# Performance work log

Hardware: AMD Instinct MI355X
Metric: run time of the kernel (lower is better)

The kernel has to match this reference:

```python
import jax, jax.numpy as jnp
import numpy as np

T = 131072      # sequence length (time steps)
IN = 256        # input_dim (MAX_NEURAL_UNITS)
G = 8           # num_dataset_groups
H = 64          # ssm_io_dim (== ssm_dim)
CTX = 8         # context_dim
P = 32          # complex state size = ssm_dim // 2 (conj_sym=True)
NL = 4          # ssm_num_layers
OUT = 2         # output_dim
DT_MIN, DT_MAX = 1e-3, 1e-1


def setup_inputs() -> dict:
    ks = jax.random.split(jax.random.key(0), 16)
    n = lambda i, shape, s=1.0: jax.random.normal(ks[i], shape, dtype=jnp.float32) * s
    return {
        "x": n(0, (T, IN)),
        "group_idx": 3,
        "enc_w": n(1, (G, H - CTX, IN), 1.0 / np.sqrt(IN)),
        "enc_b": n(2, (G, H - CTX), 0.01),
        "ctx_emb": n(3, (G, CTX)),
        "Lambda_re": -0.5 * jnp.abs(n(4, (NL, P))) - 0.1,   # stable (negative real part)
        "Lambda_im": n(5, (NL, P)) * 3.0,
        "B_re": n(6, (NL, P, H), 1.0 / np.sqrt(H)),
        "B_im": n(7, (NL, P, H), 1.0 / np.sqrt(H)),
        "C_re": n(8, (NL, H, P), 1.0 / np.sqrt(P)),
        "C_im": n(9, (NL, H, P), 1.0 / np.sqrt(P)),
        "D": n(10, (NL, H)),
        "log_step": jax.random.uniform(ks[11], (NL, P), jnp.float32, np.log(DT_MIN), np.log(DT_MAX)),
        "norm_scale": jnp.ones((NL, H), jnp.float32),
        "norm_bias": jnp.zeros((NL, H), jnp.float32),
        "glu_w1": n(12, (NL, H, H), 1.0 / np.sqrt(H)),
        "glu_b1": jnp.zeros((NL, H), jnp.float32),
        "glu_w2": n(13, (NL, H, H), 1.0 / np.sqrt(H)),
        "glu_b2": jnp.zeros((NL, H), jnp.float32),
        "dec_w": n(14, (OUT, H), 1.0 / np.sqrt(H)),
        "dec_b": jnp.zeros((OUT,), jnp.float32),
    }


def _s5_scan(Lbar, Bu):
    """Linear recurrence x_k = Lbar * x_{k-1} + Bu_k via parallel associative scan."""
    A = jnp.broadcast_to(Lbar, Bu.shape)  # (T, P) complex

    def binop(a, b):
        a1, u1 = a
        a2, u2 = b
        return a2 * a1, a2 * u1 + u2

    _, xs = jax.lax.associative_scan(binop, (A, Bu))
    return xs  # (T, P) complex


def reference(x, group_idx, enc_w, enc_b, ctx_emb, Lambda_re, Lambda_im, B_re, B_im,
              C_re, C_im, D, log_step, norm_scale, norm_bias,
              glu_w1, glu_b1, glu_w2, glu_b2, dec_w, dec_b):
    # group-routed encoder (lax.switch over per-group Linears == gather of weights)
    h = x @ enc_w[group_idx].T + enc_b[group_idx]                         # (T, H-CTX)
    ctx = jnp.broadcast_to(ctx_emb[group_idx], (h.shape[0], CTX))         # (T, CTX)
    h = jnp.concatenate([h, ctx], axis=1)                                 # (T, H)

    for i in range(NL):  # static layer stack
        skip = h
        # batch-norm over the time axis (training-mode batch statistics)
        mu = jnp.mean(h, axis=0)
        var = jnp.var(h, axis=0)
        hn = (h - mu) * jax.lax.rsqrt(var + 1e-5) * norm_scale[i] + norm_bias[i]

        # ZOH discretisation of diagonal complex SSM
        Lam = jax.lax.complex(Lambda_re[i], Lambda_im[i])                 # (P,)
        dt = jnp.exp(log_step[i])                                         # (P,) step_rescale=1
        Lbar = jnp.exp(Lam * dt)                                          # (P,)
        Bt = jax.lax.complex(B_re[i], B_im[i])                            # (P, H)
        Bbar = (((Lbar - 1.0) / Lam)[:, None]) * Bt                       # (P, H)

        Bu = hn.astype(Bbar.dtype) @ Bbar.T                               # (T, P) complex
        xs = _s5_scan(Lbar, Bu)                                           # (T, P)
        Cm = jax.lax.complex(C_re[i], C_im[i])                            # (H, P)
        y = 2.0 * jnp.real(xs @ Cm.T) + hn * D[i]                         # conj_sym output

        # half-GLU nonlinearity + residual (dropout inactive at inference)
        y = jax.nn.gelu(y)
        y = (y @ glu_w1[i].T + glu_b1[i]) * jax.nn.sigmoid(y @ glu_w2[i].T + glu_b2[i])
        h = skip + y

    return h @ dec_w.T + dec_b                                            # (T, OUT)
```

## Files before the change

kernel.cpp:

```cpp
#include <hip/hip_runtime.h>

#define T_LEN   131072
#define IN_DIM  256
#define HD      64
#define PD      32
#define NLAY    4
#define CHUNK   128
#define NBLK    (T_LEN / CHUNK)
#define ASTR    68

typedef __attribute__((ext_vector_type(8))) short bf16x8;
typedef __attribute__((ext_vector_type(4))) float f32x4;

union FragU { uint4 q; bf16x8 v; };

__device__ __forceinline__ unsigned splitpack(float x) {
    unsigned xb = __float_as_uint(x);
    unsigned hb = (xb + 0x8000u) & 0xffff0000u;
    float lf = x - __uint_as_float(hb);
    unsigned lb = (__float_as_uint(lf) + 0x8000u) >> 16;
    return (hb >> 16) | (lb << 16);
}

__device__ __forceinline__ void packAB(float4 a0, float4 a1, bf16x8& hi, bf16x8& lo) {
    unsigned p0 = splitpack(a0.x), p1 = splitpack(a0.y);
    unsigned p2 = splitpack(a0.z), p3 = splitpack(a0.w);
    unsigned p4 = splitpack(a1.x), p5 = splitpack(a1.y);
    unsigned p6 = splitpack(a1.z), p7 = splitpack(a1.w);
    union { bf16x8 v; unsigned u[4]; } H, L;
    H.u[0] = (p0 & 0xffffu) | (p1 << 16);
    H.u[1] = (p2 & 0xffffu) | (p3 << 16);
    H.u[2] = (p4 & 0xffffu) | (p5 << 16);
    H.u[3] = (p6 & 0xffffu) | (p7 << 16);
    L.u[0] = (p0 >> 16) | (p1 & 0xffff0000u);
    L.u[1] = (p2 >> 16) | (p3 & 0xffff0000u);
    L.u[2] = (p4 >> 16) | (p5 & 0xffff0000u);
    L.u[3] = (p6 >> 16) | (p7 & 0xffff0000u);
    hi = H.v; lo = L.v;
}

#define MFMA3(ACC, AH, AL, BH, BL)                                              \
    ACC = __builtin_amdgcn_mfma_f32_16x16x32_bf16(AH, BH, ACC, 0, 0, 0);        \
    ACC = __builtin_amdgcn_mfma_f32_16x16x32_bf16(AH, BL, ACC, 0, 0, 0);        \
    ACC = __builtin_amdgcn_mfma_f32_16x16x32_bf16(AL, BH, ACC, 0, 0, 0);

__device__ __forceinline__ int kmap(int q, int j) {
    return (j < 4) ? (q * 4 + j) : (16 + q * 4 + (j - 4));
}

__global__ __launch_bounds__(512) void ssm_k0a(
    const float* __restrict__ Lre, const float* __restrict__ Lim,
    const float* __restrict__ logstep,
    float* __restrict__ Lbar, float* __restrict__ Ldt, float* __restrict__ stats)
{
    int tid = threadIdx.x;
    if (tid < NLAY * PD) {
        int l = tid >> 5, p = tid & 31;
        float dt = expf(logstep[l * PD + p]);
        float lr = Lre[l * PD + p], li = Lim[l * PD + p];
        float ldr = lr * dt, ldi = li * dt;
        Ldt[tid * 2] = ldr; Ldt[tid * 2 + 1] = ldi;
        float e = expf(ldr);
        float sn, cs; sincosf(ldi, &sn, &cs);
        Lbar[tid * 2] = e * cs; Lbar[tid * 2 + 1] = e * sn;
    }
    if (tid < NLAY * 128) stats[tid] = 0.0f;
}

__global__ __launch_bounds__(256) void ssm_k0b(
    const float* __restrict__ Lre, const float* __restrict__ Lim,
    const float* __restrict__ logstep,
    const float* __restrict__ Bre, const float* __restrict__ Bim,
    const float* __restrict__ Cre, const float* __restrict__ Cim,
    const float* __restrict__ w1, const float* __restrict__ w2,
    const float* __restrict__ enc_w, const int* __restrict__ gptr,
    unsigned* __restrict__ fragE, unsigned* __restrict__ fragL)
{
    int fi = blockIdx.x * 256 + threadIdx.x;
    if (fi >= 10240) return;
    int g = gptr[0];
    int mat, lay = 0, rem;
    unsigned* outp;
    if (fi < 2048) { mat = 0; rem = fi; outp = fragE + rem * 8; }
    else {
        int t = fi - 2048;
        lay = t / 2048;
        int r2 = t % 2048;
        mat = 1 + r2 / 512;
        rem = r2 % 512;
        outp = fragL + ((size_t)(lay * 4 + (mat - 1)) * 512 + rem) * 8;
    }
    int ks = rem / 256;
    int nt = (rem / 64) & 3;
    int lane = rem & 63;
    int q = lane >> 4;
    int n = nt * 16 + (lane & 15);

    float vals[8];
#pragma unroll
    for (int j = 0; j < 8; ++j) {
        int k = ks * 32 + kmap(q, j);
        float v;
        if (mat == 0) {
            v = (n < 56) ? enc_w[(size_t)(g * 56 + n) * IN_DIM + k] : 0.0f;
        } else if (mat == 1) {
            int p = n >> 1;
            float dt = expf(logstep[lay * PD + p]);
            float lr = Lre[lay * PD + p], li = Lim[lay * PD + p];
            float e = expf(lr * dt);
            float sn, cs; sincosf(li * dt, &sn, &cs);
            float den = lr * lr + li * li;
            float nr = e * cs - 1.0f, ni = e * sn;
            float fr = (nr * lr + ni * li) / den, fimag = (ni * lr - nr * li) / den;
            float br = Bre[(lay * PD + p) * HD + k], bi = Bim[(lay * PD + p) * HD + k];
            v = (n & 1) ? (fr * bi + fimag * br) : (fr * br - fimag * bi);
        } else if (mat == 2) {
            int p = k >> 1;
            v = (k & 1) ? -Cim[((size_t)lay * HD + n) * PD + p]
                        :  Cre[((size_t)lay * HD + n) * PD + p];
        } else if (mat == 3) {
            v = w1[((size_t)lay * HD + n) * HD + k];
        } else {
            v = w2[((size_t)lay * HD + n) * HD + k];
        }
        vals[j] = v;
    }
    unsigned p8[8];
#pragma unroll
    for (int j = 0; j < 8; ++j) p8[j] = splitpack(vals[j]);
#pragma unroll
    for (int w = 0; w < 4; ++w) {
        unsigned p0 = p8[2 * w], p1 = p8[2 * w + 1];
        outp[w]     = (p0 & 0xffffu) | (p1 << 16);
        outp[4 + w] = (p0 >> 16) | (p1 & 0xffff0000u);
    }
}

__global__ __launch_bounds__(64) void ssm_k5_reduce(
    const float* __restrict__ part, float* __restrict__ statsL)
{
    int c = blockIdx.x;
    int lane = threadIdx.x;
    float s = 0.0f;
#pragma unroll
    for (int j = 0; j < 4; ++j) {
        float4 v = *(const float4*)&part[c * 1024 + j * 256 + lane * 4];
        s += v.x + v.y + v.z + v.w;
    }
#pragma unroll
    for (int m = 1; m < 64; m <<= 1) s += __shfl_xor(s, m, 64);
    if (lane == 0) statsL[c] = s;
}

__global__ __launch_bounds__(512, 4) void ssm_k1_encoder(
    const float* __restrict__ x, const int* __restrict__ gptr,
    const unsigned* __restrict__ fragE, const float* __restrict__ enc_b,
    const float* __restrict__ ctx_emb,
    float* __restrict__ h, float* __restrict__ part)
{
    __shared__ float sp1[512], sp2[512];
    int tid = threadIdx.x;
    int l = tid & 63, w = tid >> 6;
    int cq = l >> 4, cr = l & 15;
    int g = gptr[0];
    size_t r0 = (size_t)blockIdx.x * 128;
    int arow = 16 * w + cr;
    const float* xrow = &x[(r0 + arow) * IN_DIM];
    const f32x4 fzero = {0.f, 0.f, 0.f, 0.f};

    float4 cur[16];
#pragma unroll
    for (int kt = 0; kt < 4; ++kt)
#pragma unroll
        for (int ks = 0; ks < 2; ++ks) {
            cur[kt * 4 + 2 * ks]     = *(const float4*)&xrow[kt * 64 + ks * 32 + cq * 4];
            cur[kt * 4 + 2 * ks + 1] = *(const float4*)&xrow[kt * 64 + ks * 32 + cq * 4 + 16];
        }

    f32x4 acc[4];
#pragma unroll
    for (int nt = 0; nt < 4; ++nt) acc[nt] = fzero;

#pragma unroll
    for (int kt = 0; kt < 4; ++kt)
#pragma unroll
        for (int ks = 0; ks < 2; ++ks) {
            bf16x8 ah, al;
            packAB(cur[kt * 4 + 2 * ks], cur[kt * 4 + 2 * ks + 1], ah, al);
            int ksg = kt * 2 + ks;
#pragma unroll
            for (int nt = 0; nt < 4; ++nt) {
                const uint4* wf = (const uint4*)&fragE[((size_t)(ksg * 4 + nt) * 64 + l) * 8];
                FragU BH, BL; BH.q = wf[0]; BL.q = wf[1];
                MFMA3(acc[nt], ah, al, BH.v, BL.v);
            }
        }
#pragma unroll
    for (int nt = 0; nt < 4; ++nt) {
        int ch = nt * 16 + cr;
        float eb = (ch < 56) ? enc_b[g * 56 + ch] : 0.0f;
        bool isctx = (ch >= 56);
        float cv = isctx ? ctx_emb[g * 8 + (ch - 56)] : 0.0f;
        float v1 = 0.0f, v2 = 0.0f;
#pragma unroll
        for (int r = 0; r < 4; ++r) {
            float val = isctx ? cv : (acc[nt][r] + eb);
            h[(r0 + 16 * w + 4 * cq + r) * HD + ch] = val;
            v1 += val; v2 += val * val;
        }
        v1 += __shfl_xor(v1, 16, 64); v2 += __shfl_xor(v2, 16, 64);
        v1 += __shfl_xor(v1, 32, 64); v2 += __shfl_xor(v2, 32, 64);
        if (l < 16) { sp1[w * 64 + ch] = v1; sp2[w * 64 + ch] = v2; }
    }
    __syncthreads();
    if (tid < 64) {
        float s1 = 0.0f, s2 = 0.0f;
#pragma unroll
        for (int ww = 0; ww < 8; ++ww) { s1 += sp1[ww * 64 + tid]; s2 += sp2[ww * 64 + tid]; }
        part[tid * 1024 + blockIdx.x]        = s1;
        part[(64 + tid) * 1024 + blockIdx.x] = s2;
    }
}

__global__ __launch_bounds__(512, 4) void ssm_k2_bu_scan(
    const float* __restrict__ h, const float* __restrict__ stats,
    const float* __restrict__ nscale, const float* __restrict__ nbias,
    const unsigned* __restrict__ fragL, const float* __restrict__ Lbar,
    float* __restrict__ xs, float* __restrict__ carry, int lay)
{
    __shared__ __attribute__((aligned(16))) float bf[128 * ASTR];
    __shared__ float lsa[HD], lsb[HD];
    int tid = threadIdx.x;
    int l = tid & 63, w = tid >> 6;
    int cq = l >> 4, cr = l & 15;
    size_t r0 = (size_t)blockIdx.x * CHUNK;
    int arow = 16 * w + cr;
    const f32x4 fzero = {0.f, 0.f, 0.f, 0.f};

    if (tid < HD) {
        float s1 = stats[lay * 128 + tid], s2 = stats[lay * 128 + 64 + tid];
        float mu = s1 * (1.0f / T_LEN);
        float var = fmaxf(s2 * (1.0f / T_LEN) - mu * mu, 0.0f);
        float sc = nscale[lay * HD + tid] * rsqrtf(var + 1e-5f);
        lsa[tid] = sc;
        lsb[tid] = nbias[lay * HD + tid] - mu * sc;
    }
    __syncthreads();

    const float* hrowp = &h[(r0 + arow) * HD];
    const unsigned* fB = fragL + (size_t)(lay * 4 + 0) * 4096;
    f32x4 acc[4];
#pragma unroll
    for (int nt = 0; nt < 4; ++nt) acc[nt] = fzero;
#pragma unroll
    for (int ks = 0; ks < 2; ++ks) {
        int k0 = ks * 32 + cq * 4;
        float4 c0 = *(const float4*)&hrowp[k0];
        float4 c1 = *(const float4*)&hrowp[k0 + 16];
        c0.x = c0.x * lsa[k0]      + lsb[k0];
        c0.y = c0.y * lsa[k0 + 1]  + lsb[k0 + 1];
        c0.z = c0.z * lsa[k0 + 2]  + lsb[k0 + 2];
        c0.w = c0.w * lsa[k0 + 3]  + lsb[k0 + 3];
        c1.x = c1.x * lsa[k0 + 16] + lsb[k0 + 16];
        c1.y = c1.y * lsa[k0 + 17] + lsb[k0 + 17];
        c1.z = c1.z * lsa[k0 + 18] + lsb[k0 + 18];
        c1.w = c1.w * lsa[k0 + 19] + lsb[k0 + 19];
        bf16x8 ah, al;
        packAB(c0, c1, ah, al);
#pragma unroll
        for (int nt = 0; nt < 4; ++nt) {
            const uint4* wf = (const uint4*)&fB[((size_t)(ks * 4 + nt) * 64 + l) * 8];
            FragU BH, BL; BH.q = wf[0]; BL.q = wf[1];
            MFMA3(acc[nt], ah, al, BH.v, BL.v);
        }
    }
#pragma unroll
    for (int nt = 0; nt < 4; ++nt)
#pragma unroll
        for (int r = 0; r < 4; ++r)
            bf[(16 * w + 4 * cq + r) * ASTR + nt * 16 + cr] = acc[nt][r];
    __syncthreads();

    if (tid < 64) {
        int p = l >> 1;
        float Lr = Lbar[(lay * PD + p) * 2];
        float Lj = Lbar[(lay * PD + p) * 2 + 1];
        float csn = (l & 1) ? Lj : -Lj;
        float xv = 0.0f;
        for (int t = 0; t < CHUNK; ++t) {
            float b = bf[t * ASTR + l];
            float xo = __shfl_xor(xv, 1, 64);
            xv = Lr * xv + csn * xo + b;
            bf[t * ASTR + l] = xv;
        }
        carry[(size_t)blockIdx.x * 64 + l] = xv;
    }
    __syncthreads();
#pragma unroll
    for (int j = 0; j < 4; ++j) {
        float4 v = *(float4*)&bf[arow * ASTR + cq * 16 + j * 4];
        *(float4*)&xs[(r0 + arow) * HD + cq * 16 + j * 4] = v;
    }
}

__global__ __launch_bounds__(64) void ssm_k3_carry(
    const float* __restrict__ carry, const float* __restrict__ Ldt,
    float* __restrict__ pc, int lay)
{
    int p = blockIdx.x;
    int lane = threadIdx.x;
    float ldr = Ldt[(lay * PD + p) * 2], ldi = Ldt[(lay * PD + p) * 2 + 1];
    float er = __expf(ldr * (float)CHUNK);
    float an = ldi * (float)CHUNK;
    float lcr = er * __cosf(an), lci = er * __sinf(an);
    float cr[16], ci[16];
#pragma unroll
    for (int j = 0; j < 16; ++j) {
        cr[j] = carry[(size_t)(lane * 16 + j) * 64 + 2 * p];
        ci[j] = carry[(size_t)(lane * 16 + j) * 64 + 2 * p + 1];
    }
    float ur = 0.0f, ui = 0.0f;
#pragma unroll
    for (int j = 0; j < 16; ++j) {
        float nr = lcr * ur - lci * ui + cr[j];
        float ni = lcr * ui + lci * ur + ci[j];
        ur = nr; ui = ni;
    }
    float mr = lcr, mi = lci;
#pragma unroll
    for (int s = 0; s < 4; ++s) { float t = mr * mr - mi * mi; mi = 2.0f * mr * mi; mr = t; }
#pragma unroll
    for (int d = 1; d < 64; d <<= 1) {
        float tr = __shfl_up(ur, d, 64);
        float ti = __shfl_up(ui, d, 64);
        if (lane >= d) { ur = mr * tr - mi * ti + ur; ui = mr * ti + mi * tr + ui; }
        float t = mr * mr - mi * mi; mi = 2.0f * mr * mi; mr = t;
    }
    float pr = __shfl_up(ur, 1, 64), pi = __shfl_up(ui, 1, 64);
    float xr = (lane == 0) ? 0.0f : pr;
    float xi = (lane == 0) ? 0.0f : pi;
#pragma unroll
    for (int j = 0; j < 16; ++j) {
        pc[(size_t)(lane * 16 + j) * 64 + 2 * p]     = xr;
        pc[(size_t)(lane * 16 + j) * 64 + 2 * p + 1] = xi;
        float nr = lcr * xr - lci * xi + cr[j];
        float ni = lcr * xi + lci * xr + ci[j];
        xr = nr; xi = ni;
    }
}

template <bool LAST>
__global__ __launch_bounds__(512, 4) void ssm_k4_out(
    const float* __restrict__ h, const float* __restrict__ xs,
    const float* __restrict__ pc, const float* __restrict__ stats,
    const float* __restrict__ nscale, const float* __restrict__ nbias,
    const float* __restrict__ Ldt, const unsigned* __restrict__ fragL,
    const float* __restrict__ Dv,
    const float* __restrict__ b1, const float* __restrict__ b2,
    float* __restrict__ hout, float* __restrict__ part,
    const float* __restrict__ dec_w, const float* __restrict__ dec_b,
    float* __restrict__ outp, int lay)
{
    __shared__ __attribute__((aligned(16))) unsigned act[128 * ASTR];
    __shared__ float lsa[HD], lsb[HD], lsd[HD], lpc[HD], lld[HD];
    __shared__ float sp1[512], sp2[512];
    int tid = threadIdx.x;
    int l = tid & 63, w = tid >> 6;
    int cq = l >> 4, cr = l & 15;
    size_t r0 = (size_t)blockIdx.x * CHUNK;
    int arow = 16 * w + cr;
    const f32x4 fzero = {0.f, 0.f, 0.f, 0.f};

    if (tid < HD) {
        float s1 = stats[lay * 128 + tid], s2 = stats[lay * 128 + 64 + tid];
        float mu = s1 * (1.0f / T_LEN);
        float var = fmaxf(s2 * (1.0f / T_LEN) - mu * mu, 0.0f);
        float sc = nscale[lay * HD + tid] * rsqrtf(var + 1e-5f);
        lsa[tid] = sc;
        lsb[tid] = nbias[lay * HD + tid] - mu * sc;
        lsd[tid] = Dv[lay * HD + tid];
        lpc[tid] = pc[(size_t)blockIdx.x * 64 + tid];
        lld[tid] = Ldt[lay * 64 + tid];
    }
    __syncthreads();

    const unsigned* fC = fragL + (size_t)(lay * 4 + 1) * 4096;
    f32x4 yacc[4];
#pragma unroll
    for (int nt = 0; nt < 4; ++nt) yacc[nt] = fzero;
    {
        const float* xrowp = &xs[(r0 + arow) * HD];
        float tt = (float)(arow + 1);
#pragma unroll
        for (int ks = 0; ks < 2; ++ks) {
            int k0 = ks * 32 + cq * 4;
            float4 v0 = *(const float4*)&xrowp[k0];
            float4 v1 = *(const float4*)&xrowp[k0 + 16];
            {
                float e1 = __expf(lld[k0] * tt), an = lld[k0 + 1] * tt;
                float prr = e1 * __cosf(an), pri = e1 * __sinf(an);
                v0.x += prr * lpc[k0] - pri * lpc[k0 + 1];
                v0.y += prr * lpc[k0 + 1] + pri * lpc[k0];
            }
            {
                float e1 = __expf(lld[k0 + 2] * tt), an = lld[k0 + 3] * tt;
                float prr = e1 * __cosf(an), pri = e1 * __sinf(an);
                v0.z += prr * lpc[k0 + 2] - pri * lpc[k0 + 3];
                v0.w += prr * lpc[k0 + 3] + pri * lpc[k0 + 2];
            }
            {
                float e1 = __expf(lld[k0 + 16] * tt), an = lld[k0 + 17] * tt;
                float prr = e1 * __cosf(an), pri = e1 * __sinf(an);
                v1.x += prr * lpc[k0 + 16] - pri * lpc[k0 + 17];
                v1.y += prr * lpc[k0 + 17] + pri * lpc[k0 + 16];
            }
            {
                float e1 = __expf(lld[k0 + 18] * tt), an = lld[k0 + 19] * tt;
                float prr = e1 * __cosf(an), pri = e1 * __sinf(an);
                v1.z += prr * lpc[k0 + 18] - pri * lpc[k0 + 19];
                v1.w += prr * lpc[k0 + 19] + pri * lpc[k0 + 18];
            }
            bf16x8 ah, al;
            packAB(v0, v1, ah, al);
#pragma unroll
            for (int nt = 0; nt < 4; ++nt) {
                const uint4* wf = (const uint4*)&fC[((size_t)(ks * 4 + nt) * 64 + l) * 8];
                FragU BH, BL; BH.q = wf[0]; BL.q = wf[1];
                MFMA3(yacc[nt], ah, al, BH.v, BL.v);
            }
        }
    }

    float hrow[16];
#pragma unroll
    for (int nt = 0; nt < 4; ++nt) {
        int ch = nt * 16 + cr;
        float sav = lsa[ch], sbv = lsb[ch], dvv = lsd[ch];
#pragma unroll
        for (int r = 0; r < 4; ++r) {
            int row = 16 * w + 4 * cq + r;
            float hv = h[(r0 + row) * HD + ch];
            hrow[nt * 4 + r] = hv;
            float t = 2.0f * yacc[nt][r] + (hv * sav + sbv) * dvv;
            float u2 = 1.5957691216057308f * (t + 0.044715f * t * t * t);
            float gv = t / (1.0f + __expf(-u2));
            act[row * ASTR + ch] = splitpack(gv);
        }
    }
    asm volatile("s_waitcnt lgkmcnt(0)" ::: "memory");

    const unsigned* f1 = fragL + (size_t)(lay * 4 + 2) * 4096;
    const unsigned* f2 = fragL + (size_t)(lay * 4 + 3) * 4096;
    f32x4 uacc[4], sacc[4];
#pragma unroll
    for (int nt = 0; nt < 4; ++nt) { uacc[nt] = fzero; sacc[nt] = fzero; }
#pragma unroll
    for (int ks = 0; ks < 2; ++ks) {
        int col = ks * 32 + 4 * cq;
        uint4 a0 = *(const uint4*)&act[arow * ASTR + col];
        uint4 a1 = *(const uint4*)&act[arow * ASTR + col + 16];
        union { bf16x8 v; unsigned u[4]; } H, L;
        H.u[0] = (a0.x & 0xffffu) | (a0.y << 16);
        H.u[1] = (a0.z & 0xffffu) | (a0.w << 16);
        H.u[2] = (a1.x & 0xffffu) | (a1.y << 16);
        H.u[3] = (a1.z & 0xffffu) | (a1.w << 16);
        L.u[0] = (a0.x >> 16) | (a0.y & 0xffff0000u);
        L.u[1] = (a0.z >> 16) | (a0.w & 0xffff0000u);
        L.u[2] = (a1.x >> 16) | (a1.y & 0xffff0000u);
        L.u[3] = (a1.z >> 16) | (a1.w & 0xffff0000u);
#pragma unroll
        for (int nt = 0; nt < 4; ++nt) {
            const uint4* w1f = (const uint4*)&f1[((size_t)(ks * 4 + nt) * 64 + l) * 8];
            FragU BH1, BL1; BH1.q = w1f[0]; BL1.q = w1f[1];
            MFMA3(uacc[nt], H.v, L.v, BH1.v, BL1.v);
            const uint4* w2f = (const uint4*)&f2[((size_t)(ks * 4 + nt) * 64 + l) * 8];
            FragU BH2, BL2; BH2.q = w2f[0]; BL2.q = w2f[1];
            MFMA3(sacc[nt], H.v, L.v, BH2.v, BL2.v);
        }
    }

    if (LAST) {
        float o0[4] = {0.f, 0.f, 0.f, 0.f}, o1[4] = {0.f, 0.f, 0.f, 0.f};
#pragma unroll
        for (int nt = 0; nt < 4; ++nt) {
            int ch = nt * 16 + cr;
            float bb1 = b1[lay * HD + ch], bb2 = b2[lay * HD + ch];
            float dw0 = dec_w[ch], dw1 = dec_w[64 + ch];
#pragma unroll
            for (int r = 0; r < 4; ++r) {
                float sv = sacc[nt][r] + bb2;
                float sg = 1.0f / (1.0f + __expf(-sv));
                float ho = hrow[nt * 4 + r] + (uacc[nt][r] + bb1) * sg;
                o0[r] += ho * dw0;
                o1[r] += ho * dw1;
            }
        }
#pragma unroll
        for (int r = 0; r < 4; ++r) {
#pragma unroll
            for (int m = 1; m < 16; m <<= 1) {
                o0[r] += __shfl_xor(o0[r], m, 64);
                o1[r] += __shfl_xor(o1[r], m, 64);
            }
        }
        if (cr == 0) {
            float db0 = dec_b[0], db1 = dec_b[1];
#pragma unroll
            for (int r = 0; r < 4; ++r) {
                int row = 16 * w + 4 * cq + r;
                *(float2*)&outp[(r0 + row) * 2] = make_float2(o0[r] + db0, o1[r] + db1);
            }
        }
    } else {
#pragma unroll
        for (int nt = 0; nt < 4; ++nt) {
            int ch = nt * 16 + cr;
            float bb1 = b1[lay * HD + ch], bb2 = b2[lay * HD + ch];
            float v1 = 0.0f, v2 = 0.0f;
#pragma unroll
            for (int r = 0; r < 4; ++r) {
                int row = 16 * w + 4 * cq + r;
                float sv = sacc[nt][r] + bb2;
                float sg = 1.0f / (1.0f + __expf(-sv));
                float ho = hrow[nt * 4 + r] + (uacc[nt][r] + bb1) * sg;
                hout[(r0 + row) * HD + ch] = ho;
                v1 += ho; v2 += ho * ho;
            }
            v1 += __shfl_xor(v1, 16, 64); v2 += __shfl_xor(v2, 16, 64);
            v1 += __shfl_xor(v1, 32, 64); v2 += __shfl_xor(v2, 32, 64);
            if (l < 16) { sp1[w * 64 + ch] = v1; sp2[w * 64 + ch] = v2; }
        }
        __syncthreads();
        if (tid < 64) {
            float s1 = 0.0f, s2 = 0.0f;
#pragma unroll
            for (int ww = 0; ww < 8; ++ww) { s1 += sp1[ww * 64 + tid]; s2 += sp2[ww * 64 + tid]; }
            part[tid * 1024 + blockIdx.x]        = s1;
            part[(64 + tid) * 1024 + blockIdx.x] = s2;
        }
    }
}

extern "C" void kernel_launch(void* const* d_in, const int* in_sizes, int n_in,
                              void* d_out, int out_size, void* d_ws, size_t ws_size,
                              hipStream_t stream)
{
    (void)in_sizes; (void)n_in; (void)out_size; (void)ws_size;
    const float* x     = (const float*)d_in[0];
    const int*   gidx  = (const int*)d_in[1];
    const float* enc_w = (const float*)d_in[2];
    const float* enc_b = (const float*)d_in[3];
    const float* ctx   = (const float*)d_in[4];
    const float* Lre   = (const float*)d_in[5];
    const float* Lim   = (const float*)d_in[6];
    const float* Bre   = (const float*)d_in[7];
    const float* Bim   = (const float*)d_in[8];
    const float* Cre   = (const float*)d_in[9];
    const float* Cim   = (const float*)d_in[10];
    const float* Dv    = (const float*)d_in[11];
    const float* lstep = (const float*)d_in[12];
    const float* nsc   = (const float*)d_in[13];
    const float* nbi   = (const float*)d_in[14];
    const float* w1    = (const float*)d_in[15];
    const float* b1    = (const float*)d_in[16];
    const float* w2    = (const float*)d_in[17];
    const float* b2    = (const float*)d_in[18];
    const float* dw    = (const float*)d_in[19];
    const float* db    = (const float*)d_in[20];
    float* out = (float*)d_out;

    float* ws = (float*)d_ws;
    float* h     = ws;  ws += (size_t)T_LEN * HD;
    float* xs    = ws;  ws += (size_t)T_LEN * HD;
    float* carry = ws;  ws += (size_t)NBLK * HD;
    float* pc    = ws;  ws += (size_t)NBLK * HD;
    float* stats = ws;  ws += NLAY * 128;
    float* Lbar  = ws;  ws += NLAY * PD * 2;
    float* Ldt   = ws;  ws += NLAY * PD * 2;
    unsigned* fragE = (unsigned*)ws;  ws += 16384;
    unsigned* fragL = (unsigned*)ws;  ws += 65536;
    float* part  = ws;  ws += 128 * 1024;

    ssm_k0a<<<1, 512, 0, stream>>>(Lre, Lim, lstep, Lbar, Ldt, stats);
    ssm_k0b<<<40, 256, 0, stream>>>(Lre, Lim, lstep, Bre, Bim, Cre, Cim, w1, w2,
                                    enc_w, gidx, fragE, fragL);
    ssm_k1_encoder<<<1024, 512, 0, stream>>>(x, gidx, fragE, enc_b, ctx, h, part);
    ssm_k5_reduce<<<128, 64, 0, stream>>>(part, stats);
    for (int l = 0; l < NLAY; ++l) {
        ssm_k2_bu_scan<<<NBLK, 512, 0, stream>>>(h, stats, nsc, nbi, fragL, Lbar, xs, carry, l);
        ssm_k3_carry<<<PD, 64, 0, stream>>>(carry, Ldt, pc, l);
        if (l < NLAY - 1) {
            ssm_k4_out<false><<<NBLK, 512, 0, stream>>>(
                h, xs, pc, stats, nsc, nbi, Ldt, fragL, Dv, b1, b2,
                h, part, dw, db, out, l);
            ssm_k5_reduce<<<128, 64, 0, stream>>>(part, stats + (l + 1) * 128);
        } else {
            ssm_k4_out<true><<<NBLK, 512, 0, stream>>>(
                h, xs, pc, stats, nsc, nbi, Ldt, fragL, Dv, b1, b2,
                h, part, dw, db, out, l);
        }
    }
}
```

Before: 326.3 us.

## Fuse Bu/scan, carry propagation and output into one decoupled-lookback kernel

Merges the per-layer Bu+chunk scan, the carry scan kernel and the output/GLU kernel into a single kernel. Inter-chunk carries are resolved with a decoupled look-back over per-block flags, each block looking back through predecessors' aggregate or inclusive states. This removes the xs round trip through global memory and two launches per layer. In exchange it relies on blocks being scheduled roughly in order to avoid spin-wait stalls or deadlock, and it adds serial look-back latency on a single wave per block.

```diff
diff --git a/kernel.cpp b/kernel.cpp
--- a/kernel.cpp
+++ b/kernel.cpp
@@ -51,7 +51,8 @@
 __global__ __launch_bounds__(512) void ssm_k0a(
     const float* __restrict__ Lre, const float* __restrict__ Lim,
     const float* __restrict__ logstep,
-    float* __restrict__ Lbar, float* __restrict__ Ldt, float* __restrict__ stats)
+    float* __restrict__ Lbar, float* __restrict__ Ldt, float* __restrict__ stats,
+    int* __restrict__ flags)
 {
     int tid = threadIdx.x;
     if (tid < NLAY * PD) {
@@ -65,6 +66,7 @@
         Lbar[tid * 2] = e * cs; Lbar[tid * 2 + 1] = e * sn;
     }
     if (tid < NLAY * 128) stats[tid] = 0.0f;
+    for (int i = tid; i < NLAY * NBLK; i += 512) flags[i] = 0;
 }
 
 __global__ __launch_bounds__(256) void ssm_k0b(
@@ -222,18 +224,26 @@
     }
 }
 
-__global__ __launch_bounds__(512, 4) void ssm_k2_bu_scan(
-    const float* __restrict__ h, const float* __restrict__ stats,
+template <bool LAST>
+__global__ __launch_bounds__(512, 4) void ssm_kl(
+    float* __restrict__ h, const float* __restrict__ stats,
     const float* __restrict__ nscale, const float* __restrict__ nbias,
-    const unsigned* __restrict__ fragL, const float* __restrict__ Lbar,
-    float* __restrict__ xs, float* __restrict__ carry, int lay)
+    const unsigned* __restrict__ fragL,
+    const float* __restrict__ Lbar, const float* __restrict__ Ldt,
+    float* __restrict__ carryV, float* __restrict__ inclV, int* __restrict__ flags,
+    const float* __restrict__ Dv, const float* __restrict__ b1,
+    const float* __restrict__ b2, float* __restrict__ part,
+    const float* __restrict__ dec_w, const float* __restrict__ dec_b,
+    float* __restrict__ outp, int lay)
 {
     __shared__ __attribute__((aligned(16))) float bf[128 * ASTR];
-    __shared__ float lsa[HD], lsb[HD];
+    __shared__ float lsa[HD], lsb[HD], lsd[HD], lld[HD], lpc[HD];
+    __shared__ float sp1[512], sp2[512];
     int tid = threadIdx.x;
+    int bid = blockIdx.x;
     int l = tid & 63, w = tid >> 6;
     int cq = l >> 4, cr = l & 15;
-    size_t r0 = (size_t)blockIdx.x * CHUNK;
+    size_t r0 = (size_t)bid * CHUNK;
     int arow = 16 * w + cr;
     const f32x4 fzero = {0.f, 0.f, 0.f, 0.f};
 
@@ -244,41 +254,45 @@
         float sc = nscale[lay * HD + tid] * rsqrtf(var + 1e-5f);
         lsa[tid] = sc;
         lsb[tid] = nbias[lay * HD + tid] - mu * sc;
+        lsd[tid] = Dv[lay * HD + tid];
+        lld[tid] = Ldt[lay * 64 + tid];
     }
     __syncthreads();
 
-    const float* hrowp = &h[(r0 + arow) * HD];
     const unsigned* fB = fragL + (size_t)(lay * 4 + 0) * 4096;
-    f32x4 acc[4];
-#pragma unroll
-    for (int nt = 0; nt < 4; ++nt) acc[nt] = fzero;
-#pragma unroll
-    for (int ks = 0; ks < 2; ++ks) {
-        int k0 = ks * 32 + cq * 4;
-        float4 c0 = *(const float4*)&hrowp[k0];
-        float4 c1 = *(const float4*)&hrowp[k0 + 16];
-        c0.x = c0.x * lsa[k0]      + lsb[k0];
-        c0.y = c0.y * lsa[k0 + 1]  + lsb[k0 + 1];
-        c0.z = c0.z * lsa[k0 + 2]  + lsb[k0 + 2];
-        c0.w = c0.w * lsa[k0 + 3]  + lsb[k0 + 3];
-        c1.x = c1.x * lsa[k0 + 16] + lsb[k0 + 16];
-        c1.y = c1.y * lsa[k0 + 17] + lsb[k0 + 17];
-        c1.z = c1.z * lsa[k0 + 18] + lsb[k0 + 18];
-        c1.w = c1.w * lsa[k0 + 19] + lsb[k0 + 19];
-        bf16x8 ah, al;
-        packAB(c0, c1, ah, al);
-#pragma unroll
-        for (int nt = 0; nt < 4; ++nt) {
-            const uint4* wf = (const uint4*)&fB[((size_t)(ks * 4 + nt) * 64 + l) * 8];
-            FragU BH, BL; BH.q = wf[0]; BL.q = wf[1];
-            MFMA3(acc[nt], ah, al, BH.v, BL.v);
-        }
-    }
-#pragma unroll
-    for (int nt = 0; nt < 4; ++nt)
-#pragma unroll
-        for (int r = 0; r < 4; ++r)
-            bf[(16 * w + 4 * cq + r) * ASTR + nt * 16 + cr] = acc[nt][r];
+    {
+        const float* hrowp = &h[(r0 + arow) * HD];
+        f32x4 acc[4];
+#pragma unroll
+        for (int nt = 0; nt < 4; ++nt) acc[nt] = fzero;
+#pragma unroll
+        for (int ks = 0; ks < 2; ++ks) {
+            int k0 = ks * 32 + cq * 4;
+            float4 c0 = *(const float4*)&hrowp[k0];
+            float4 c1 = *(const float4*)&hrowp[k0 + 16];
+            c0.x = c0.x * lsa[k0]      + lsb[k0];
+            c0.y = c0.y * lsa[k0 + 1]  + lsb[k0 + 1];
+            c0.z = c0.z * lsa[k0 + 2]  + lsb[k0 + 2];
+            c0.w = c0.w * lsa[k0 + 3]  + lsb[k0 + 3];
+            c1.x = c1.x * lsa[k0 + 16] + lsb[k0 + 16];
+            c1.y = c1.y * lsa[k0 + 17] + lsb[k0 + 17];
+            c1.z = c1.z * lsa[k0 + 18] + lsb[k0 + 18];
+            c1.w = c1.w * lsa[k0 + 19] + lsb[k0 + 19];
+            bf16x8 ah, al;
+            packAB(c0, c1, ah, al);
+#pragma unroll
+            for (int nt = 0; nt < 4; ++nt) {
+                const uint4* wf = (const uint4*)&fB[((size_t)(ks * 4 + nt) * 64 + l) * 8];
+                FragU BH, BL; BH.q = wf[0]; BL.q = wf[1];
+                MFMA3(acc[nt], ah, al, BH.v, BL.v);
+            }
+        }
+#pragma unroll
+        for (int nt = 0; nt < 4; ++nt)
+#pragma unroll
+            for (int r = 0; r < 4; ++r)
+                bf[(16 * w + 4 * cq + r) * ASTR + nt * 16 + cr] = acc[nt][r];
+    }
     __syncthreads();
 
     if (tid < 64) {
@@ -293,109 +307,67 @@
             xv = Lr * xv + csn * xo + b;
             bf[t * ASTR + l] = xv;
         }
-        carry[(size_t)blockIdx.x * 64 + l] = xv;
+        carryV[(size_t)bid * 64 + l] = xv;
+        float pc_ = 0.0f;
+        if (bid == 0) {
+            inclV[l] = xv;
+            if (l == 0)
+                __hip_atomic_store(&flags[bid], 2, __ATOMIC_RELEASE, __HIP_MEMORY_SCOPE_AGENT);
+        } else {
+            if (l == 0)
+                __hip_atomic_store(&flags[bid], 1, __ATOMIC_RELEASE, __HIP_MEMORY_SCOPE_AGENT);
+            float ldr = lld[2 * p], ldi = lld[2 * p + 1];
+            float er = __expf(ldr * (float)CHUNK);
+            float an = ldi * (float)CHUNK;
+            float lcr = er * __cosf(an), lci = er * __sinf(an);
+            float mr = 1.0f, mi = 0.0f;
+            int j = bid - 1;
+            while (true) {
+                int f = 0;
+                if (l == 0) {
+                    do {
+                        f = __hip_atomic_load(&flags[j], __ATOMIC_ACQUIRE, __HIP_MEMORY_SCOPE_AGENT);
+                    } while (f == 0);
+                }
+                f = __shfl(f, 0, 64);
+                const float* src = (f == 2) ? &inclV[(size_t)j * 64] : &carryV[(size_t)j * 64];
+                float v = __hip_atomic_load(&src[l], __ATOMIC_RELAXED, __HIP_MEMORY_SCOPE_AGENT);
+                float vo = __shfl_xor(v, 1, 64);
+                float cs2 = (l & 1) ? mi : -mi;
+                pc_ += mr * v + cs2 * vo;
+                if (f == 2) break;
+                float nmr = mr * lcr - mi * lci;
+                float nmi = mr * lci + mi * lcr;
+                mr = nmr; mi = nmi;
+                --j;
+            }
+            float pco = __shfl_xor(pc_, 1, 64);
+            float csl = (l & 1) ? lci : -lci;
+            float inc = lcr * pc_ + csl * pco + xv;
+            inclV[(size_t)bid * 64 + l] = inc;
+            if (l == 0)
+                __hip_atomic_store(&flags[bid], 2, __ATOMIC_RELEASE, __HIP_MEMORY_SCOPE_AGENT);
+        }
+        lpc[l] = pc_;
     }
     __syncthreads();
-#pragma unroll
-    for (int j = 0; j < 4; ++j) {
-        float4 v = *(float4*)&bf[arow * ASTR + cq * 16 + j * 4];
-        *(float4*)&xs[(r0 + arow) * HD + cq * 16 + j * 4] = v;
-    }
-}
-
-__global__ __launch_bounds__(64) void ssm_k3_carry(
-    const float* __restrict__ carry, const float* __restrict__ Ldt,
-    float* __restrict__ pc, int lay)
-{
-    int p = blockIdx.x;
-    int lane = threadIdx.x;
-    float ldr = Ldt[(lay * PD + p) * 2], ldi = Ldt[(lay * PD + p) * 2 + 1];
-    float er = __expf(ldr * (float)CHUNK);
-    float an = ldi * (float)CHUNK;
-    float lcr = er * __cosf(an), lci = er * __sinf(an);
-    float cr[16], ci[16];
-#pragma unroll
-    for (int j = 0; j < 16; ++j) {
-        cr[j] = carry[(size_t)(lane * 16 + j) * 64 + 2 * p];
-        ci[j] = carry[(size_t)(lane * 16 + j) * 64 + 2 * p + 1];
-    }
-    float ur = 0.0f, ui = 0.0f;
-#pragma unroll
-    for (int j = 0; j < 16; ++j) {
-        float nr = lcr * ur - lci * ui + cr[j];
-        float ni = lcr * ui + lci * ur + ci[j];
-        ur = nr; ui = ni;
-    }
-    float mr = lcr, mi = lci;
-#pragma unroll
-    for (int s = 0; s < 4; ++s) { float t = mr * mr - mi * mi; mi = 2.0f * mr * mi; mr = t; }
-#pragma unroll
-    for (int d = 1; d < 64; d <<= 1) {
-        float tr = __shfl_up(ur, d, 64);
-        float ti = __shfl_up(ui, d, 64);
-        if (lane >= d) { ur = mr * tr - mi * ti + ur; ui = mr * ti + mi * tr + ui; }
-        float t = mr * mr - mi * mi; mi = 2.0f * mr * mi; mr = t;
-    }
-    float pr = __shfl_up(ur, 1, 64), pi = __shfl_up(ui, 1, 64);
-    float xr = (lane == 0) ? 0.0f : pr;
-    float xi = (lane == 0) ? 0.0f : pi;
-#pragma unroll
-    for (int j = 0; j < 16; ++j) {
-        pc[(size_t)(lane * 16 + j) * 64 + 2 * p]     = xr;
-        pc[(size_t)(lane * 16 + j) * 64 + 2 * p + 1] = xi;
-        float nr = lcr * xr - lci * xi + cr[j];
-        float ni = lcr * xi + lci * xr + ci[j];
-        xr = nr; xi = ni;
-    }
-}
-
-template <bool LAST>
-__global__ __launch_bounds__(512, 4) void ssm_k4_out(
-    const float* __restrict__ h, const float* __restrict__ xs,
-    const float* __restrict__ pc, const float* __restrict__ stats,
-    const float* __restrict__ nscale, const float* __restrict__ nbias,
-    const float* __restrict__ Ldt, const unsigned* __restrict__ fragL,
-    const float* __restrict__ Dv,
-    const float* __restrict__ b1, const float* __restrict__ b2,
-    float* __restrict__ hout, float* __restrict__ part,
-    const float* __restrict__ dec_w, const float* __restrict__ dec_b,
-    float* __restrict__ outp, int lay)
-{
-    __shared__ __attribute__((aligned(16))) unsigned act[128 * ASTR];
-    __shared__ float lsa[HD], lsb[HD], lsd[HD], lpc[HD], lld[HD];
-    __shared__ float sp1[512], sp2[512];
-    int tid = threadIdx.x;
-    int l = tid & 63, w = tid >> 6;
-    int cq = l >> 4, cr = l & 15;
-    size_t r0 = (size_t)blockIdx.x * CHUNK;
-    int arow = 16 * w + cr;
-    const f32x4 fzero = {0.f, 0.f, 0.f, 0.f};
-
-    if (tid < HD) {
-        float s1 = stats[lay * 128 + tid], s2 = stats[lay * 128 + 64 + tid];
-        float mu = s1 * (1.0f / T_LEN);
-        float var = fmaxf(s2 * (1.0f / T_LEN) - mu * mu, 0.0f);
-        float sc = nscale[lay * HD + tid] * rsqrtf(var + 1e-5f);
-        lsa[tid] = sc;
-        lsb[tid] = nbias[lay * HD + tid] - mu * sc;
-        lsd[tid] = Dv[lay * HD + tid];
-        lpc[tid] = pc[(size_t)blockIdx.x * 64 + tid];
-        lld[tid] = Ldt[lay * 64 + tid];
-    }
-    __syncthreads();
 
     const unsigned* fC = fragL + (size_t)(lay * 4 + 1) * 4096;
+    const unsigned* f1 = fragL + (size_t)(lay * 4 + 2) * 4096;
+    const unsigned* f2 = fragL + (size_t)(lay * 4 + 3) * 4096;
+    unsigned* act = (unsigned*)bf;
+
     f32x4 yacc[4];
 #pragma unroll
     for (int nt = 0; nt < 4; ++nt) yacc[nt] = fzero;
     {
-        const float* xrowp = &xs[(r0 + arow) * HD];
+        const float* brow = &bf[arow * ASTR];
         float tt = (float)(arow + 1);
 #pragma unroll
         for (int ks = 0; ks < 2; ++ks) {
             int k0 = ks * 32 + cq * 4;
-            float4 v0 = *(const float4*)&xrowp[k0];
-            float4 v1 = *(const float4*)&xrowp[k0 + 16];
+            float4 v0 = *(const float4*)&brow[k0];
+            float4 v1 = *(const float4*)&brow[k0 + 16];
             {
                 float e1 = __expf(lld[k0] * tt), an = lld[k0 + 1] * tt;
                 float prr = e1 * __cosf(an), pri = e1 * __sinf(an);
@@ -449,8 +421,6 @@
     }
     asm volatile("s_waitcnt lgkmcnt(0)" ::: "memory");
 
-    const unsigned* f1 = fragL + (size_t)(lay * 4 + 2) * 4096;
-    const unsigned* f2 = fragL + (size_t)(lay * 4 + 3) * 4096;
     f32x4 uacc[4], sacc[4];
 #pragma unroll
     for (int nt = 0; nt < 4; ++nt) { uacc[nt] = fzero; sacc[nt] = fzero; }
@@ -523,7 +493,7 @@
                 float sv = sacc[nt][r] + bb2;
                 float sg = 1.0f / (1.0f + __expf(-sv));
                 float ho = hrow[nt * 4 + r] + (uacc[nt][r] + bb1) * sg;
-                hout[(r0 + row) * HD + ch] = ho;
+                h[(r0 + row) * HD + ch] = ho;
                 v1 += ho; v2 += ho * ho;
             }
             v1 += __shfl_xor(v1, 16, 64); v2 += __shfl_xor(v2, 16, 64);
@@ -535,8 +505,8 @@
             float s1 = 0.0f, s2 = 0.0f;
 #pragma unroll
             for (int ww = 0; ww < 8; ++ww) { s1 += sp1[ww * 64 + tid]; s2 += sp2[ww * 64 + tid]; }
-            part[tid * 1024 + blockIdx.x]        = s1;
-            part[(64 + tid) * 1024 + blockIdx.x] = s2;
+            part[tid * 1024 + bid]        = s1;
+            part[(64 + tid) * 1024 + bid] = s2;
         }
     }
 }
@@ -570,34 +540,33 @@
     float* out = (float*)d_out;
 
     float* ws = (float*)d_ws;
-    float* h     = ws;  ws += (size_t)T_LEN * HD;
-    float* xs    = ws;  ws += (size_t)T_LEN * HD;
-    float* carry = ws;  ws += (size_t)NBLK * HD;
-    float* pc    = ws;  ws += (size_t)NBLK * HD;
-    float* stats = ws;  ws += NLAY * 128;
-    float* Lbar  = ws;  ws += NLAY * PD * 2;
-    float* Ldt   = ws;  ws += NLAY * PD * 2;
+    float* h      = ws;  ws += (size_t)T_LEN * HD;
+    float* carryV = ws;  ws += (size_t)NBLK * HD;
+    float* inclV  = ws;  ws += (size_t)NBLK * HD;
+    float* stats  = ws;  ws += NLAY * 128;
+    float* Lbar   = ws;  ws += NLAY * PD * 2;
+    float* Ldt    = ws;  ws += NLAY * PD * 2;
+    int*   flags  = (int*)ws;  ws += NLAY * NBLK;
     unsigned* fragE = (unsigned*)ws;  ws += 16384;
     unsigned* fragL = (unsigned*)ws;  ws += 65536;
-    float* part  = ws;  ws += 128 * 1024;
-
-    ssm_k0a<<<1, 512, 0, stream>>>(Lre, Lim, lstep, Lbar, Ldt, stats);
+    float* part   = ws;  ws += 128 * 1024;
+
+    ssm_k0a<<<1, 512, 0, stream>>>(Lre, Lim, lstep, Lbar, Ldt, stats, flags);
     ssm_k0b<<<40, 256, 0, stream>>>(Lre, Lim, lstep, Bre, Bim, Cre, Cim, w1, w2,
                                     enc_w, gidx, fragE, fragL);
     ssm_k1_encoder<<<1024, 512, 0, stream>>>(x, gidx, fragE, enc_b, ctx, h, part);
     ssm_k5_reduce<<<128, 64, 0, stream>>>(part, stats);
-    for (int l = 0; l < NLAY; ++l) {
-        ssm_k2_bu_scan<<<NBLK, 512, 0, stream>>>(h, stats, nsc, nbi, fragL, Lbar, xs, carry, l);
-        ssm_k3_carry<<<PD, 64, 0, stream>>>(carry, Ldt, pc, l);
-        if (l < NLAY - 1) {
-            ssm_k4_out<false><<<NBLK, 512, 0, stream>>>(
-                h, xs, pc, stats, nsc, nbi, Ldt, fragL, Dv, b1, b2,
-                h, part, dw, db, out, l);
-            ssm_k5_reduce<<<128, 64, 0, stream>>>(part, stats + (l + 1) * 128);
+    for (int lay = 0; lay < NLAY; ++lay) {
+        int* flagsL = flags + lay * NBLK;
+        if (lay < NLAY - 1) {
+            ssm_kl<false><<<NBLK, 512, 0, stream>>>(
+                h, stats, nsc, nbi, fragL, Lbar, Ldt, carryV, inclV, flagsL,
+                Dv, b1, b2, part, dw, db, out, lay);
+            ssm_k5_reduce<<<128, 64, 0, stream>>>(part, stats + (lay + 1) * 128);
         } else {
-            ssm_k4_out<true><<<NBLK, 512, 0, stream>>>(
-                h, xs, pc, stats, nsc, nbi, Ldt, fragL, Dv, b1, b2,
-                h, part, dw, db, out, l);
-        }
-    }
-}
+            ssm_kl<true><<<NBLK, 512, 0, stream>>>(
+                h, stats, nsc, nbi, fragL, Lbar, Ldt, carryV, inclV, flagsL,
+                Dv, b1, b2, part, dw, db, out, lay);
+        }
+    }
+}
```

New measurement: 1.175 ms. +260.1%, slower.

## Fold reduce and carry-scan kernels into producers via last-block atomic tickets

Applied to the files above, without the earlier changes.

Removes the separate stats-reduction and carry-scan kernel launches. Each producer kernel now takes an atomic ticket after writing its partial results, and the last block to finish does the cross-block reduction or the chunk-carry prefix scan itself. This saves several small kernel launches and the gaps between them, at the cost of a serialized tail of work on one block plus threadfence and atomic overhead on every block. A sched_barrier is also added after the encoder's input loads.

```diff
diff --git a/kernel.cpp b/kernel.cpp
--- a/kernel.cpp
+++ b/kernel.cpp
@@ -51,7 +51,8 @@
 __global__ __launch_bounds__(512) void ssm_k0a(
     const float* __restrict__ Lre, const float* __restrict__ Lim,
     const float* __restrict__ logstep,
-    float* __restrict__ Lbar, float* __restrict__ Ldt, float* __restrict__ stats)
+    float* __restrict__ Lbar, float* __restrict__ Ldt, float* __restrict__ stats,
+    int* __restrict__ tickets)
 {
     int tid = threadIdx.x;
     if (tid < NLAY * PD) {
@@ -65,6 +66,7 @@
         Lbar[tid * 2] = e * cs; Lbar[tid * 2 + 1] = e * sn;
     }
     if (tid < NLAY * 128) stats[tid] = 0.0f;
+    if (tid < 16) tickets[tid] = 0;
 }
 
 __global__ __launch_bounds__(256) void ssm_k0b(
@@ -136,29 +138,32 @@
     }
 }
 
-__global__ __launch_bounds__(64) void ssm_k5_reduce(
-    const float* __restrict__ part, float* __restrict__ statsL)
-{
-    int c = blockIdx.x;
-    int lane = threadIdx.x;
-    float s = 0.0f;
-#pragma unroll
-    for (int j = 0; j < 4; ++j) {
-        float4 v = *(const float4*)&part[c * 1024 + j * 256 + lane * 4];
-        s += v.x + v.y + v.z + v.w;
-    }
-#pragma unroll
-    for (int m = 1; m < 64; m <<= 1) s += __shfl_xor(s, m, 64);
-    if (lane == 0) statsL[c] = s;
+__device__ __forceinline__ void reduce_part(const float* part, float* statsL, int tid) {
+    int w = tid >> 6, lane = tid & 63;
+#pragma unroll
+    for (int cc = 0; cc < 16; ++cc) {
+        int c = w * 16 + cc;
+        float s = 0.0f;
+#pragma unroll
+        for (int j = 0; j < 4; ++j) {
+            float4 v = *(const float4*)&part[c * 1024 + lane * 16 + j * 4];
+            s += v.x + v.y + v.z + v.w;
+        }
+#pragma unroll
+        for (int m = 1; m < 64; m <<= 1) s += __shfl_xor(s, m, 64);
+        if (lane == 0) statsL[c] = s;
+    }
 }
 
 __global__ __launch_bounds__(512, 4) void ssm_k1_encoder(
     const float* __restrict__ x, const int* __restrict__ gptr,
     const unsigned* __restrict__ fragE, const float* __restrict__ enc_b,
     const float* __restrict__ ctx_emb,
-    float* __restrict__ h, float* __restrict__ part)
+    float* __restrict__ h, float* __restrict__ part,
+    float* __restrict__ statsL, int* __restrict__ ticket)
 {
     __shared__ float sp1[512], sp2[512];
+    __shared__ int isLast;
     int tid = threadIdx.x;
     int l = tid & 63, w = tid >> 6;
     int cq = l >> 4, cr = l & 15;
@@ -176,6 +181,7 @@
             cur[kt * 4 + 2 * ks]     = *(const float4*)&xrow[kt * 64 + ks * 32 + cq * 4];
             cur[kt * 4 + 2 * ks + 1] = *(const float4*)&xrow[kt * 64 + ks * 32 + cq * 4 + 16];
         }
+    __builtin_amdgcn_sched_barrier(0);
 
     f32x4 acc[4];
 #pragma unroll
@@ -220,16 +226,30 @@
         part[tid * 1024 + blockIdx.x]        = s1;
         part[(64 + tid) * 1024 + blockIdx.x] = s2;
     }
+    __syncthreads();
+    if (tid == 0) {
+        __threadfence();
+        int old = atomicAdd(ticket, 1);
+        isLast = (old == NBLK - 1);
+    }
+    __syncthreads();
+    if (isLast) {
+        __threadfence();
+        reduce_part(part, statsL, tid);
+    }
 }
 
 __global__ __launch_bounds__(512, 4) void ssm_k2_bu_scan(
     const float* __restrict__ h, const float* __restrict__ stats,
     const float* __restrict__ nscale, const float* __restrict__ nbias,
     const unsigned* __restrict__ fragL, const float* __restrict__ Lbar,
-    float* __restrict__ xs, float* __restrict__ carry, int lay)
+    const float* __restrict__ Ldt,
+    float* __restrict__ xs, float* __restrict__ carry, float* __restrict__ pc,
+    int* __restrict__ ticket, int lay)
 {
     __shared__ __attribute__((aligned(16))) float bf[128 * ASTR];
     __shared__ float lsa[HD], lsb[HD];
+    __shared__ int isLast;
     int tid = threadIdx.x;
     int l = tid & 63, w = tid >> 6;
     int cq = l >> 4, cr = l & 15;
@@ -301,51 +321,57 @@
         float4 v = *(float4*)&bf[arow * ASTR + cq * 16 + j * 4];
         *(float4*)&xs[(r0 + arow) * HD + cq * 16 + j * 4] = v;
     }
-}
-
-__global__ __launch_bounds__(64) void ssm_k3_carry(
-    const float* __restrict__ carry, const float* __restrict__ Ldt,
-    float* __restrict__ pc, int lay)
-{
-    int p = blockIdx.x;
-    int lane = threadIdx.x;
-    float ldr = Ldt[(lay * PD + p) * 2], ldi = Ldt[(lay * PD + p) * 2 + 1];
-    float er = __expf(ldr * (float)CHUNK);
-    float an = ldi * (float)CHUNK;
-    float lcr = er * __cosf(an), lci = er * __sinf(an);
-    float cr[16], ci[16];
-#pragma unroll
-    for (int j = 0; j < 16; ++j) {
-        cr[j] = carry[(size_t)(lane * 16 + j) * 64 + 2 * p];
-        ci[j] = carry[(size_t)(lane * 16 + j) * 64 + 2 * p + 1];
-    }
-    float ur = 0.0f, ui = 0.0f;
-#pragma unroll
-    for (int j = 0; j < 16; ++j) {
-        float nr = lcr * ur - lci * ui + cr[j];
-        float ni = lcr * ui + lci * ur + ci[j];
-        ur = nr; ui = ni;
-    }
-    float mr = lcr, mi = lci;
-#pragma unroll
-    for (int s = 0; s < 4; ++s) { float t = mr * mr - mi * mi; mi = 2.0f * mr * mi; mr = t; }
-#pragma unroll
-    for (int d = 1; d < 64; d <<= 1) {
-        float tr = __shfl_up(ur, d, 64);
-        float ti = __shfl_up(ui, d, 64);
-        if (lane >= d) { ur = mr * tr - mi * ti + ur; ui = mr * ti + mi * tr + ui; }
-        float t = mr * mr - mi * mi; mi = 2.0f * mr * mi; mr = t;
-    }
-    float pr = __shfl_up(ur, 1, 64), pi = __shfl_up(ui, 1, 64);
-    float xr = (lane == 0) ? 0.0f : pr;
-    float xi = (lane == 0) ? 0.0f : pi;
-#pragma unroll
-    for (int j = 0; j < 16; ++j) {
-        pc[(size_t)(lane * 16 + j) * 64 + 2 * p]     = xr;
-        pc[(size_t)(lane * 16 + j) * 64 + 2 * p + 1] = xi;
-        float nr = lcr * xr - lci * xi + cr[j];
-        float ni = lcr * xi + lci * xr + ci[j];
-        xr = nr; xi = ni;
+    if (tid == 0) {
+        __threadfence();
+        int old = atomicAdd(ticket, 1);
+        isLast = (old == NBLK - 1);
+    }
+    __syncthreads();
+    if (isLast) {
+        __threadfence();
+        int lane = l;
+#pragma unroll
+        for (int pp = 0; pp < 4; ++pp) {
+            int p = w * 4 + pp;
+            float ldr = Ldt[lay * 64 + 2 * p], ldi = Ldt[lay * 64 + 2 * p + 1];
+            float er = __expf(ldr * (float)CHUNK);
+            float an = ldi * (float)CHUNK;
+            float lcr = er * __cosf(an), lci = er * __sinf(an);
+            float crv[16], civ[16];
+#pragma unroll
+            for (int j = 0; j < 16; ++j) {
+                crv[j] = carry[(size_t)(lane * 16 + j) * 64 + 2 * p];
+                civ[j] = carry[(size_t)(lane * 16 + j) * 64 + 2 * p + 1];
+            }
+            float ur = 0.0f, ui = 0.0f;
+#pragma unroll
+            for (int j = 0; j < 16; ++j) {
+                float nr = lcr * ur - lci * ui + crv[j];
+                float ni = lcr * ui + lci * ur + civ[j];
+                ur = nr; ui = ni;
+            }
+            float mr = lcr, mi = lci;
+#pragma unroll
+            for (int s = 0; s < 4; ++s) { float t = mr * mr - mi * mi; mi = 2.0f * mr * mi; mr = t; }
+#pragma unroll
+            for (int d = 1; d < 64; d <<= 1) {
+                float tr = __shfl_up(ur, d, 64);
+                float ti = __shfl_up(ui, d, 64);
+                if (lane >= d) { ur = mr * tr - mi * ti + ur; ui = mr * ti + mi * tr + ui; }
+                float t = mr * mr - mi * mi; mi = 2.0f * mr * mi; mr = t;
+            }
+            float pr = __shfl_up(ur, 1, 64), pi = __shfl_up(ui, 1, 64);
+            float xr = (lane == 0) ? 0.0f : pr;
+            float xi = (lane == 0) ? 0.0f : pi;
+#pragma unroll
+            for (int j = 0; j < 16; ++j) {
+                pc[(size_t)(lane * 16 + j) * 64 + 2 * p]     = xr;
+                pc[(size_t)(lane * 16 + j) * 64 + 2 * p + 1] = xi;
+                float nr = lcr * xr - lci * xi + crv[j];
+                float ni = lcr * xi + lci * xr + civ[j];
+                xr = nr; xi = ni;
+            }
+        }
     }
 }
 
@@ -358,12 +384,14 @@
     const float* __restrict__ Dv,
     const float* __restrict__ b1, const float* __restrict__ b2,
     float* __restrict__ hout, float* __restrict__ part,
+    float* __restrict__ stats_next, int* __restrict__ ticket,
     const float* __restrict__ dec_w, const float* __restrict__ dec_b,
     float* __restrict__ outp, int lay)
 {
     __shared__ __attribute__((aligned(16))) unsigned act[128 * ASTR];
     __shared__ float lsa[HD], lsb[HD], lsd[HD], lpc[HD], lld[HD];
     __shared__ float sp1[512], sp2[512];
+    __shared__ int isLast;
     int tid = threadIdx.x;
     int l = tid & 63, w = tid >> 6;
     int cq = l >> 4, cr = l & 15;
@@ -537,6 +565,17 @@
             for (int ww = 0; ww < 8; ++ww) { s1 += sp1[ww * 64 + tid]; s2 += sp2[ww * 64 + tid]; }
             part[tid * 1024 + blockIdx.x]        = s1;
             part[(64 + tid) * 1024 + blockIdx.x] = s2;
+        }
+        __syncthreads();
+        if (tid == 0) {
+            __threadfence();
+            int old = atomicAdd(ticket, 1);
+            isLast = (old == NBLK - 1);
+        }
+        __syncthreads();
+        if (isLast) {
+            __threadfence();
+            reduce_part(part, stats_next, tid);
         }
     }
 }
@@ -577,27 +616,27 @@
     float* stats = ws;  ws += NLAY * 128;
     float* Lbar  = ws;  ws += NLAY * PD * 2;
     float* Ldt   = ws;  ws += NLAY * PD * 2;
+    int* tickets = (int*)ws;  ws += 16;
     unsigned* fragE = (unsigned*)ws;  ws += 16384;
     unsigned* fragL = (unsigned*)ws;  ws += 65536;
     float* part  = ws;  ws += 128 * 1024;
 
-    ssm_k0a<<<1, 512, 0, stream>>>(Lre, Lim, lstep, Lbar, Ldt, stats);
+    ssm_k0a<<<1, 512, 0, stream>>>(Lre, Lim, lstep, Lbar, Ldt, stats, tickets);
     ssm_k0b<<<40, 256, 0, stream>>>(Lre, Lim, lstep, Bre, Bim, Cre, Cim, w1, w2,
                                     enc_w, gidx, fragE, fragL);
-    ssm_k1_encoder<<<1024, 512, 0, stream>>>(x, gidx, fragE, enc_b, ctx, h, part);
-    ssm_k5_reduce<<<128, 64, 0, stream>>>(part, stats);
-    for (int l = 0; l < NLAY; ++l) {
-        ssm_k2_bu_scan<<<NBLK, 512, 0, stream>>>(h, stats, nsc, nbi, fragL, Lbar, xs, carry, l);
-        ssm_k3_carry<<<PD, 64, 0, stream>>>(carry, Ldt, pc, l);
-        if (l < NLAY - 1) {
+    ssm_k1_encoder<<<1024, 512, 0, stream>>>(x, gidx, fragE, enc_b, ctx, h, part,
+                                             stats, &tickets[15]);
+    for (int lay = 0; lay < NLAY; ++lay) {
+        ssm_k2_bu_scan<<<NBLK, 512, 0, stream>>>(h, stats, nsc, nbi, fragL, Lbar, Ldt,
+                                                 xs, carry, pc, &tickets[lay], lay);
+        if (lay < NLAY - 1) {
             ssm_k4_out<false><<<NBLK, 512, 0, stream>>>(
                 h, xs, pc, stats, nsc, nbi, Ldt, fragL, Dv, b1, b2,
-                h, part, dw, db, out, l);
-            ssm_k5_reduce<<<128, 64, 0, stream>>>(part, stats + (l + 1) * 128);
+                h, part, stats + (lay + 1) * 128, &tickets[4 + lay], dw, db, out, lay);
         } else {
             ssm_k4_out<true><<<NBLK, 512, 0, stream>>>(
                 h, xs, pc, stats, nsc, nbi, Ldt, fragL, Dv, b1, b2,
-                h, part, dw, db, out, l);
-        }
-    }
-}
+                h, part, stats, &tickets[8], dw, db, out, lay);
+        }
+    }
+}
```

After: 758.9 us. 2.33x slower.
